# Performance work log

Measured on AMD Instinct MI355X. Metric: run time of the kernel, lower is better.

Reference implementation:

```python
import jax, jax.numpy as jnp
import numpy as np

N_NODE, N_USER = 100000, 30000
N_REL, N_BASIS = 8, 30
EMB, OUT = 32, 32
E = 1600000
BATCH = 16384
H1, H2, H3 = 64, 32, 16
NEG_SLOPE = 0.2


def setup_inputs() -> dict:
    key = jax.random.key(0)
    ks = jax.random.split(key, 20)
    g = lambda k, shape: jax.random.normal(k, shape, dtype=jnp.float32) * 0.05
    inp = {
        "x_ids": jnp.arange(N_NODE, dtype=jnp.int64 if jax.config.jax_enable_x64 else jnp.int32),
        "edge_index": jax.random.randint(ks[0], (2, E), 0, N_NODE),
        "edge_type": jax.random.randint(ks[1], (E,), 0, N_REL),
        "users": jax.random.randint(ks[2], (BATCH,), 0, N_USER),
        "bundles": jax.random.randint(ks[3], (BATCH,), 0, N_NODE),
        # parameters
        "emb": g(ks[4], (N_NODE, EMB)),
        "basis": g(ks[5], (N_BASIS, EMB, OUT)),
        "weight": g(ks[6], (N_REL, N_BASIS)),
        "att": g(ks[7], (N_REL, 2 * OUT)),
        "root": g(ks[8], (EMB, OUT)),
        "bias": jnp.zeros((OUT,), jnp.float32),
        "W1": g(ks[9], (2 * OUT, H1)), "b1": jnp.zeros((H1,), jnp.float32),
        "W2": g(ks[10], (H1, H2)), "b2": jnp.zeros((H2,), jnp.float32),
        "W3": g(ks[11], (H2, H3)), "b3": jnp.zeros((H3,), jnp.float32),
        "Wo": g(ks[12], (H3, 1)), "bo": jnp.zeros((1,), jnp.float32),
    }
    return inp


def _tgcn_fwd(x_ids, edge_index, edge_type, users, bundles,
              emb, basis, weight, att, root, bias,
              W1, b1, W2, b2, W3, b3, Wo, bo):
    N = emb.shape[0]
    R = weight.shape[0]
    O = basis.shape[2]
    x = emb[x_ids]                                   # (N, F) embedding lookup
    # basis decomposition: (R, F, O)
    w = (weight @ basis.reshape(N_BASIS, -1)).reshape(R, EMB, O)
    # transform every node under every relation once, then gather per edge
    xh = jnp.einsum('nf,rfo->nro', x, w)             # (N, R, O)
    src, dst = edge_index[0], edge_index[1]          # j (source), i (target)
    h_i = xh[dst, edge_type]                         # (E, O)
    h_j = xh[src, edge_type]                         # (E, O)
    a = att[edge_type]                               # (E, 2O)
    alpha = (h_i * a[:, :O]).sum(-1) + (h_j * a[:, O:]).sum(-1)
    alpha = jax.nn.leaky_relu(alpha, NEG_SLOPE)
    # segment softmax keyed by (target node, relation)
    seg_key = dst * R + edge_type
    n_seg = N * R
    amax = jax.ops.segment_max(alpha, seg_key, num_segments=n_seg)
    ex = jnp.exp(alpha - amax[seg_key])
    denom = jax.ops.segment_sum(ex, seg_key, num_segments=n_seg)
    alpha = ex / (denom[seg_key] + 1e-16)
    # scatter-add weighted messages into target nodes
    agg = jax.ops.segment_sum(h_j * alpha[:, None], dst, num_segments=N)
    h = jax.nn.relu(agg + x @ root + bias)           # update + ReLU
    z = jnp.concatenate([h[users], h[bundles]], axis=1)  # (B, 2O)
    z = jax.nn.relu(z @ W1 + b1)
    z = jax.nn.relu(z @ W2 + b2)
    z = jax.nn.relu(z @ W3 + b3)
    return z @ Wo + bo                               # (B, 1) logits


def reference(x_ids, edge_index, edge_type, users, bundles,
              emb, basis, weight, att, root, bias,
              W1, b1, W2, b2, W3, b3, Wo, bo):
    return _tgcn_fwd(x_ids, edge_index, edge_type, users, bundles,
                     emb, basis, weight, att, root, bias,
                     W1, b1, W2, b2, W3, b3, Wo, bo)
```

## Files before the change

### kernel.cpp

```cpp
#include <hip/hip_runtime.h>
#include <hip/hip_bf16.h>

#define N_NODE 100000
#define N_REL  8
#define EMB    32
#define OUT    32
#define N_BASIS 30
#define E_EDGE 1600000
#define BATCH  16384
#define H1 64
#define H2 32
#define H3 16
#define NEG_SLOPE 0.2f

#define BSH   8
#define NBKT  391
#define BCAP  5120
#define PCH   2048

#define K5T   128

#define NPB   32
#define NTILES (N_NODE / NPB)
#define K1GRID 782
#define XSS   36
#define RTS   36


__global__ __launch_bounds__(256) void k0f(const float* __restrict__ weight,
                                           const float* __restrict__ basis,
                                           const float* __restrict__ att,
                                           float* __restrict__ w,
                                           float* __restrict__ wa,
                                           unsigned* __restrict__ bcnt) {
    __shared__ float wl[N_REL * EMB * OUT];
    int t = threadIdx.x;
    for (int i = t; i < N_REL * EMB * OUT; i += 256) {
        int r = i >> 10, fo = i & 1023;
        float acc = 0.f;
        #pragma unroll
        for (int b = 0; b < N_BASIS; b++)
            acc = fmaf(weight[r * N_BASIS + b], basis[b * (EMB * OUT) + fo], acc);
        wl[i] = acc;
        w[i] = acc;
    }
    __syncthreads();
    for (int i = t; i < 512; i += 256) {
        int which = i >> 8, rf = i & 255, r = rf >> 5, f = rf & 31;
        const float* wrow = wl + (r * 32 + f) * 32;
        const float* arow = att + r * 64 + which * 32;
        float acc = 0.f;
        #pragma unroll
        for (int o = 0; o < 32; o++) acc = fmaf(wrow[o], arow[o], acc);
        wa[i] = acc;
    }
    for (int i = t; i < NBKT; i += 256) bcnt[i] = 0;
}

__global__ __launch_bounds__(256) void k1x(const float* __restrict__ emb,
                                           const float* __restrict__ w,
                                           const float* __restrict__ wa,
                                           const float* __restrict__ root,
                                           const float* __restrict__ bias,
                                           unsigned short* __restrict__ xh,
                                           float* __restrict__ p_i,
                                           float* __restrict__ p_j,
                                           float* __restrict__ agg) {
    __shared__ float xs[2][NPB * XSS];
    __shared__ float rootsT[OUT * RTS];
    __shared__ float was[16 * RTS];
    __shared__ float biass[OUT];

    const int t = threadIdx.x;
    const int ro = t & 127;
    const int rhi = ro >> 5, olo = ro & 31;

    float wc0[EMB], wc1[EMB];
    #pragma unroll
    for (int f = 0; f < EMB; f++) {
        wc0[f] = w[rhi * 1024 + f * 32 + olo];
        wc1[f] = w[rhi * 1024 + 4096 + f * 32 + olo];
    }
    #pragma unroll
    for (int f = 0; f < EMB; f++) asm volatile("" : "+v"(wc0[f]), "+v"(wc1[f]));

    for (int i = t; i < EMB * OUT; i += 256) {
        int f = i >> 5, oo = i & 31;
        rootsT[oo * RTS + f] = root[i];
    }
    for (int i = t; i < 512; i += 256) {
        int which = i >> 8, r = (i >> 5) & 7, f = i & 31;
        was[(which * 8 + r) * RTS + f] = wa[i];
    }
    if (t < OUT) biass[t] = bias[t];

    const int sn = t >> 3, sc = t & 7;
    int tile = blockIdx.x;
    {
        float4 v = ((const float4*)(emb + (size_t)tile * NPB * EMB))[t];
        *(float4*)&xs[0][sn * XSS + sc * 4] = v;
    }
    __syncthreads();

    int buf = 0;
    for (; tile < NTILES; tile += K1GRID) {
        const int ntile = tile + K1GRID;
        const bool has = ntile < NTILES;
        float4 pf;
        if (has)
            pf = ((const float4*)(emb + (size_t)ntile * NPB * EMB))[t];

        const int n0 = tile * NPB;
        const float* xb = xs[buf];

        {
            const float4* xr = (const float4*)&xb[(t >> 3) * XSS];
            const float4* wi = (const float4*)&was[(t & 7) * RTS];
            const float4* wj = (const float4*)&was[(8 + (t & 7)) * RTS];
            float ai = 0.f, aj = 0.f;
            #pragma unroll
            for (int c = 0; c < 8; c++) {
                float4 xv = xr[c];
                float4 vi = wi[c], vj = wj[c];
                ai = fmaf(xv.x, vi.x, ai); ai = fmaf(xv.y, vi.y, ai);
                ai = fmaf(xv.z, vi.z, ai); ai = fmaf(xv.w, vi.w, ai);
                aj = fmaf(xv.x, vj.x, aj); aj = fmaf(xv.y, vj.y, aj);
                aj = fmaf(xv.z, vj.z, aj); aj = fmaf(xv.w, vj.w, aj);
            }
            p_i[n0 * N_REL + t] = ai;
            p_j[n0 * N_REL + t] = aj;
        }

        {
            const int o = t & 31, ng = t >> 5;
            const float4* rt = (const float4*)&rootsT[o * RTS];
            float4 r0 = rt[0], r1 = rt[1], r2 = rt[2], r3 = rt[3];
            float4 r4 = rt[4], r5 = rt[5], r6 = rt[6], r7 = rt[7];
            float bv = biass[o];
            #pragma unroll
            for (int q = 0; q < 4; q++) {
                int n = ng * 4 + q;
                const float4* xr = (const float4*)&xb[n * XSS];
                float g = bv;
                float4 xv;
                xv = xr[0]; g = fmaf(xv.x, r0.x, g); g = fmaf(xv.y, r0.y, g);
                            g = fmaf(xv.z, r0.z, g); g = fmaf(xv.w, r0.w, g);
                xv = xr[1]; g = fmaf(xv.x, r1.x, g); g = fmaf(xv.y, r1.y, g);
                            g = fmaf(xv.z, r1.z, g); g = fmaf(xv.w, r1.w, g);
                xv = xr[2]; g = fmaf(xv.x, r2.x, g); g = fmaf(xv.y, r2.y, g);
                            g = fmaf(xv.z, r2.z, g); g = fmaf(xv.w, r2.w, g);
                xv = xr[3]; g = fmaf(xv.x, r3.x, g); g = fmaf(xv.y, r3.y, g);
                            g = fmaf(xv.z, r3.z, g); g = fmaf(xv.w, r3.w, g);
                xv = xr[4]; g = fmaf(xv.x, r4.x, g); g = fmaf(xv.y, r4.y, g);
                            g = fmaf(xv.z, r4.z, g); g = fmaf(xv.w, r4.w, g);
                xv = xr[5]; g = fmaf(xv.x, r5.x, g); g = fmaf(xv.y, r5.y, g);
                            g = fmaf(xv.z, r5.z, g); g = fmaf(xv.w, r5.w, g);
                xv = xr[6]; g = fmaf(xv.x, r6.x, g); g = fmaf(xv.y, r6.y, g);
                            g = fmaf(xv.z, r6.z, g); g = fmaf(xv.w, r6.w, g);
                xv = xr[7]; g = fmaf(xv.x, r7.x, g); g = fmaf(xv.y, r7.y, g);
                            g = fmaf(xv.z, r7.z, g); g = fmaf(xv.w, r7.w, g);
                agg[(size_t)(n0 + n) * OUT + o] = g;
            }
        }

        {
            const int half = t >> 7;
            #pragma unroll 4
            for (int s = 0; s < 16; s++) {
                int n = 2 * s + half;
                const float4* xr = (const float4*)&xb[n * XSS];
                float a0 = 0.f, a1 = 0.f;
                #pragma unroll
                for (int c = 0; c < 8; c++) {
                    float4 xv = xr[c];
                    a0 = fmaf(xv.x, wc0[4 * c + 0], a0);
                    a0 = fmaf(xv.y, wc0[4 * c + 1], a0);
                    a0 = fmaf(xv.z, wc0[4 * c + 2], a0);
                    a0 = fmaf(xv.w, wc0[4 * c + 3], a0);
                    a1 = fmaf(xv.x, wc1[4 * c + 0], a1);
                    a1 = fmaf(xv.y, wc1[4 * c + 1], a1);
                    a1 = fmaf(xv.z, wc1[4 * c + 2], a1);
                    a1 = fmaf(xv.w, wc1[4 * c + 3], a1);
                }
                __hip_bfloat16 b0 = __float2bfloat16(a0);
                __hip_bfloat16 b1 = __float2bfloat16(a1);
                unsigned short* xp = xh + (size_t)(n0 + n) * 256;
                xp[ro]       = *(unsigned short*)&b0;
                xp[ro + 128] = *(unsigned short*)&b1;
            }
        }

        if (has)
            *(float4*)&xs[buf ^ 1][sn * XSS + sc * 4] = pf;
        __syncthreads();
        buf ^= 1;
    }
}

__global__ __launch_bounds__(256) void k_part(const int* __restrict__ src,
                                              const int* __restrict__ dst,
                                              const int* __restrict__ et,
                                              unsigned* __restrict__ bcnt,
                                              unsigned* __restrict__ part) {
    __shared__ unsigned long long stage[PCH];
    __shared__ unsigned hist[NBKT], lbase[NBKT], lcur[NBKT], gbase[NBKT];
    __shared__ unsigned sc[256];
    int t = threadIdx.x;
    for (int i = t; i < NBKT; i += 256) hist[i] = 0;
    __syncthreads();
    int beg = blockIdx.x * PCH, end = min(beg + PCH, E_EDGE);
    int n = end - beg;
    int ng = n >> 2;
    int g0 = t, g1 = t + 256;
    bool has0 = g0 < ng, has1 = g1 < ng;
    int4 s0v = {}, d0v = {}, e0v = {}, s1v = {}, d1v = {}, e1v = {};
    if (has0) {
        s0v = *(const int4*)&src[beg + 4 * g0];
        d0v = *(const int4*)&dst[beg + 4 * g0];
        e0v = *(const int4*)&et[beg + 4 * g0];
    }
    if (has1) {
        s1v = *(const int4*)&src[beg + 4 * g1];
        d1v = *(const int4*)&dst[beg + 4 * g1];
        e1v = *(const int4*)&et[beg + 4 * g1];
    }
    if (has0) {
        atomicAdd(&hist[(unsigned)d0v.x >> BSH], 1u);
        atomicAdd(&hist[(unsigned)d0v.y >> BSH], 1u);
        atomicAdd(&hist[(unsigned)d0v.z >> BSH], 1u);
        atomicAdd(&hist[(unsigned)d0v.w >> BSH], 1u);
    }
    if (has1) {
        atomicAdd(&hist[(unsigned)d1v.x >> BSH], 1u);
        atomicAdd(&hist[(unsigned)d1v.y >> BSH], 1u);
        atomicAdd(&hist[(unsigned)d1v.z >> BSH], 1u);
        atomicAdd(&hist[(unsigned)d1v.w >> BSH], 1u);
    }
    __syncthreads();
    unsigned v0 = (2 * t < NBKT) ? hist[2 * t] : 0u;
    unsigned v1 = (2 * t + 1 < NBKT) ? hist[2 * t + 1] : 0u;
    unsigned s = v0 + v1;
    sc[t] = s;
    __syncthreads();
    for (int off = 1; off < 256; off <<= 1) {
        unsigned y = (t >= off) ? sc[t - off] : 0u;
        __syncthreads();
        sc[t] += y;
        __syncthreads();
    }
    unsigned ex = sc[t] - s;
    if (2 * t < NBKT)     { lbase[2 * t] = ex;          lcur[2 * t] = ex; }
    if (2 * t + 1 < NBKT) { lbase[2 * t + 1] = ex + v0; lcur[2 * t + 1] = ex + v0; }
    __syncthreads();
    #define K_PART_STAGE(dd, ss, ee) do {                                   \
        unsigned b_ = (unsigned)(dd) >> BSH;                                \
        unsigned ent_ = ((unsigned)((dd) & 255) << 20)                      \
                      | ((unsigned)(ss) << 3) | (unsigned)(ee);             \
        unsigned pos_ = atomicAdd(&lcur[b_], 1u);                           \
        stage[pos_] = ((unsigned long long)b_ << 32) | ent_; } while (0)
    if (has0) {
        K_PART_STAGE(d0v.x, s0v.x, e0v.x);
        K_PART_STAGE(d0v.y, s0v.y, e0v.y);
        K_PART_STAGE(d0v.z, s0v.z, e0v.z);
        K_PART_STAGE(d0v.w, s0v.w, e0v.w);
    }
    if (has1) {
        K_PART_STAGE(d1v.x, s1v.x, e1v.x);
        K_PART_STAGE(d1v.y, s1v.y, e1v.y);
        K_PART_STAGE(d1v.z, s1v.z, e1v.z);
        K_PART_STAGE(d1v.w, s1v.w, e1v.w);
    }
    #undef K_PART_STAGE
    __syncthreads();
    for (int i = t; i < NBKT; i += 256)
        if (hist[i]) gbase[i] = atomicAdd(&bcnt[i], hist[i]);
    __syncthreads();
    for (int i = t; i < n; i += 256) {
        unsigned long long s64 = stage[i];
        unsigned b = (unsigned)(s64 >> 32);
        unsigned ent = (unsigned)s64;
        part[b * BCAP + gbase[b] + (i - lbase[b])] = ent;
    }
}

__global__ __launch_bounds__(256) void k_sort(const unsigned* __restrict__ bcnt,
                                              const unsigned* __restrict__ part,
                                              int* __restrict__ payload,
                                              int* __restrict__ begp,
                                              int* __restrict__ endp) {
    __shared__ unsigned ent[BCAP];
    __shared__ unsigned ent2[BCAP];
    __shared__ unsigned hist[256], dbase[256], dcur[256];
    __shared__ unsigned sc[256];
    int t = threadIdx.x;
    int b = blockIdx.x;
    unsigned s0 = (unsigned)b * BCAP;
    int n = (int)bcnt[b];
    if (n > BCAP) n = BCAP;
    hist[t] = 0;
    __syncthreads();
    int n4 = n & ~3;
    for (int i = 4 * t; i < n4; i += 1024) {
        uint4 e4 = *(const uint4*)&part[s0 + i];
        ent[i + 0] = e4.x; atomicAdd(&hist[e4.x >> 20], 1u);
        ent[i + 1] = e4.y; atomicAdd(&hist[e4.y >> 20], 1u);
        ent[i + 2] = e4.z; atomicAdd(&hist[e4.z >> 20], 1u);
        ent[i + 3] = e4.w; atomicAdd(&hist[e4.w >> 20], 1u);
    }
    for (int i = n4 + t; i < n; i += 256) {
        unsigned e = part[s0 + i];
        ent[i] = e;
        atomicAdd(&hist[e >> 20], 1u);
    }
    __syncthreads();
    unsigned v = hist[t];
    sc[t] = v;
    __syncthreads();
    for (int off = 1; off < 256; off <<= 1) {
        unsigned y = (t >= off) ? sc[t - off] : 0u;
        __syncthreads();
        sc[t] += y;
        __syncthreads();
    }
    unsigned ex = sc[t] - v;
    dbase[t] = ex;
    dcur[t] = ex;
    __syncthreads();
    int d = (b << BSH) + t;
    if (d < N_NODE) {
        begp[d] = (int)(s0 + dbase[t]);
        endp[d] = (int)(s0 + dbase[t] + hist[t]);
    }
    for (int i = t; i < n; i += 256) {
        unsigned e = ent[i];
        unsigned pos = atomicAdd(&dcur[e >> 20], 1u);
        ent2[pos] = e & 0xFFFFFu;
    }
    __syncthreads();
    for (int i = 4 * t; i < n4; i += 1024) {
        uint4 o4 = { ent2[i + 0], ent2[i + 1], ent2[i + 2], ent2[i + 3] };
        *(uint4*)&payload[s0 + i] = o4;
    }
    for (int i = n4 + t; i < n; i += 256) payload[s0 + i] = (int)ent2[i];
}

__global__ __launch_bounds__(256) void k_agg(const int* __restrict__ begp,
                                             const int* __restrict__ endp,
                                             const int* __restrict__ payload,
                                             const float* __restrict__ p_i,
                                             const float* __restrict__ p_j,
                                             const unsigned short* __restrict__ xh,
                                             float* __restrict__ agg,
                                             int d0, int d1) {
    int d = d0 + blockIdx.x * 4 + (threadIdx.x >> 6);
    if (d >= d1) return;
    const int lane = threadIdx.x & 63;
    const int h = lane >> 5;
    const int o = lane & 31;
    const int beg = begp[d], end = endp[d];
    const int cnt = end - beg;
    if (cnt == 0) return;

    float pid[8];
    #pragma unroll
    for (int k = 0; k < 8; k++) pid[k] = p_i[(d << 3) | k];

    if (cnt <= 64) {
        int sr = 0, r = 0; float ev = 0.f;
        if (lane < cnt) {
            sr = payload[beg + lane];
            r = sr & 7;
            float pi = pid[0];
            #pragma unroll
            for (int k = 1; k < 8; k++) pi = (r == k) ? pid[k] : pi;
            float a = pi + p_j[sr];
            a = (a >= 0.f) ? a : NEG_SLOPE * a;
            ev = __expf(a);
        }
        float sex[8];
        #pragma unroll
        for (int k = 0; k < 8; k++) sex[k] = (r == k) ? ev : 0.f;
        #pragma unroll
        for (int k = 0; k < 8; k++) {
            #pragma unroll
            for (int m = 1; m <= 32; m <<= 1) sex[k] += __shfl_xor(sex[k], m, 64);
        }
        float de = sex[0];
        #pragma unroll
        for (int k = 1; k < 8; k++) de = (r == k) ? sex[k] : de;
        float al = ev / (de + 1e-16f);

        float w0 = 0.f, w1 = 0.f, w2 = 0.f, w3 = 0.f;
        for (int j0 = 0; j0 < cnt; j0 += 8) {
            float b0 = __shfl(al, j0 + h,     64);
            float b1 = __shfl(al, j0 + 2 + h, 64);
            float b2 = __shfl(al, j0 + 4 + h, 64);
            float b3 = __shfl(al, j0 + 6 + h, 64);
            int t0 = payload[beg + j0 + h]     & 0xFFFFF;
            int t1 = payload[beg + j0 + 2 + h] & 0xFFFFF;
            int t2 = payload[beg + j0 + 4 + h] & 0xFFFFF;
            int t3 = payload[beg + j0 + 6 + h] & 0xFFFFF;
            float x0 = __uint_as_float((unsigned)xh[((unsigned)t0 << 5) + o] << 16);
            float x1 = __uint_as_float((unsigned)xh[((unsigned)t1 << 5) + o] << 16);
            float x2 = __uint_as_float((unsigned)xh[((unsigned)t2 << 5) + o] << 16);
            float x3 = __uint_as_float((unsigned)xh[((unsigned)t3 << 5) + o] << 16);
            w0 = fmaf(b0, x0, w0); w1 = fmaf(b1, x1, w1);
            w2 = fmaf(b2, x2, w2); w3 = fmaf(b3, x3, w3);
        }
        float vv = (w0 + w1) + (w2 + w3);
        vv += __shfl_xor(vv, 32, 64);
        if (h == 0) agg[(size_t)d * OUT + o] += vv;
        return;
    }

    float sex[8] = {0.f,0.f,0.f,0.f,0.f,0.f,0.f,0.f};
    for (int i = beg + lane; i < end; i += 64) {
        int sr = payload[i];
        int r = sr & 7;
        float pi = pid[0];
        #pragma unroll
        for (int k = 1; k < 8; k++) pi = (r == k) ? pid[k] : pi;
        float a = pi + p_j[sr];
        a = (a >= 0.f) ? a : NEG_SLOPE * a;
        float ev = __expf(a);
        #pragma unroll
        for (int k = 0; k < 8; k++) sex[k] += (r == k) ? ev : 0.f;
    }
    #pragma unroll
    for (int k = 0; k < 8; k++) {
        #pragma unroll
        for (int m = 1; m <= 32; m <<= 1) sex[k] += __shfl_xor(sex[k], m, 64);
    }
    float v0 = 0.f;
    for (int c = beg; c < end; c += 64) {
        int i = c + lane;
        int sr = 0; float al = 0.f;
        if (i < end) {
            sr = payload[i];
            int r = sr & 7;
            float pi = pid[0];
            #pragma unroll
            for (int k = 1; k < 8; k++) pi = (r == k) ? pid[k] : pi;
            float a = pi + p_j[sr];
            a = (a >= 0.f) ? a : NEG_SLOPE * a;
            float ev = __expf(a);
            float de = sex[0];
            #pragma unroll
            for (int k = 1; k < 8; k++) de = (r == k) ? sex[k] : de;
            al = ev / (de + 1e-16f);
        }
        int m = min(64, end - c);
        for (int j0 = 0; j0 < m; j0 += 2) {
            int e0 = j0 + h;
            float a0 = __shfl(al, e0, 64); int s0 = __shfl(sr, e0, 64);
            if (e0 < m) {
                float xv = __uint_as_float((unsigned)xh[((unsigned)s0 << 5) + o] << 16);
                v0 = fmaf(a0, xv, v0);
            }
        }
    }
    float vv = v0;
    vv += __shfl_xor(vv, 32, 64);
    if (h == 0) agg[(size_t)d * OUT + o] += vv;
}

__global__ __launch_bounds__(K5T, 1) void k5_mlp(const int* __restrict__ users,
                                                 const int* __restrict__ bundles,
                                                 const float* __restrict__ agg,
                                                 const float* __restrict__ W1,
                                                 const float* __restrict__ b1,
                                                 const float* __restrict__ W2,
                                                 const float* __restrict__ b2,
                                                 const float* __restrict__ W3,
                                                 const float* __restrict__ b3,
                                                 const float* __restrict__ Wo,
                                                 const float* __restrict__ bo,
                                                 float* __restrict__ out) {
    __shared__ float4 W1s[2 * OUT * H1 / 4];
    __shared__ float4 W2s[H1 * H2 / 4];
    __shared__ float4 W3s[H2 * H3 / 4];
    __shared__ float b1s[H1], b2s[H2], b3s[H3], Wos[H3];
    __shared__ float bos;
    __shared__ float zs[K5T * 65];
    __shared__ float h1s[K5T * 65];
    const int t = threadIdx.x;

    const float4* W14 = (const float4*)W1;
    const float4* W24 = (const float4*)W2;
    const float4* W34 = (const float4*)W3;
    for (int i = t; i < 1024; i += K5T) W1s[i] = W14[i];
    for (int i = t; i < 512; i += K5T) W2s[i] = W24[i];
    for (int i = t; i < 128; i += K5T) W3s[i] = W34[i];
    if (t < H1) b1s[t] = b1[t];
    if (t < H2) b2s[t] = b2[t];
    if (t < H3) { b3s[t] = b3[t]; Wos[t] = Wo[t]; }
    if (t == 0) bos = bo[0];

    const int item = blockIdx.x * K5T + t;
    const int u = users[item], v = bundles[item];
    const float4* av = (const float4*)agg;
    float* zrow = &zs[t * 65];
    float* h1row = &h1s[t * 65];

    #pragma unroll
    for (int c = 0; c < 8; c++) {
        float4 x = av[(size_t)u * 8 + c];
        zrow[4 * c + 0] = fmaxf(x.x, 0.f); zrow[4 * c + 1] = fmaxf(x.y, 0.f);
        zrow[4 * c + 2] = fmaxf(x.z, 0.f); zrow[4 * c + 3] = fmaxf(x.w, 0.f);
    }
    #pragma unroll
    for (int c = 0; c < 8; c++) {
        float4 x = av[(size_t)v * 8 + c];
        zrow[32 + 4 * c + 0] = fmaxf(x.x, 0.f); zrow[32 + 4 * c + 1] = fmaxf(x.y, 0.f);
        zrow[32 + 4 * c + 2] = fmaxf(x.z, 0.f); zrow[32 + 4 * c + 3] = fmaxf(x.w, 0.f);
    }
    __syncthreads();

    #pragma unroll 4
    for (int j4 = 0; j4 < 16; j4++) {
        float a0 = b1s[4 * j4 + 0], a1 = b1s[4 * j4 + 1];
        float a2 = b1s[4 * j4 + 2], a3 = b1s[4 * j4 + 3];
        #pragma unroll 16
        for (int k = 0; k < 2 * OUT; k++) {
            float zk = zrow[k];
            float4 wv = W1s[k * 16 + j4];
            a0 = fmaf(zk, wv.x, a0); a1 = fmaf(zk, wv.y, a1);
            a2 = fmaf(zk, wv.z, a2); a3 = fmaf(zk, wv.w, a3);
        }
        h1row[4 * j4 + 0] = fmaxf(a0, 0.f); h1row[4 * j4 + 1] = fmaxf(a1, 0.f);
        h1row[4 * j4 + 2] = fmaxf(a2, 0.f); h1row[4 * j4 + 3] = fmaxf(a3, 0.f);
    }

    #pragma unroll 4
    for (int j4 = 0; j4 < 8; j4++) {
        float a0 = b2s[4 * j4 + 0], a1 = b2s[4 * j4 + 1];
        float a2 = b2s[4 * j4 + 2], a3 = b2s[4 * j4 + 3];
        #pragma unroll 16
        for (int k = 0; k < H1; k++) {
            float hk = h1row[k];
            float4 wv = W2s[k * 8 + j4];
            a0 = fmaf(hk, wv.x, a0); a1 = fmaf(hk, wv.y, a1);
            a2 = fmaf(hk, wv.z, a2); a3 = fmaf(hk, wv.w, a3);
        }
        zrow[4 * j4 + 0] = fmaxf(a0, 0.f); zrow[4 * j4 + 1] = fmaxf(a1, 0.f);
        zrow[4 * j4 + 2] = fmaxf(a2, 0.f); zrow[4 * j4 + 3] = fmaxf(a3, 0.f);
    }

    float h3v[16];
    #pragma unroll
    for (int j4 = 0; j4 < 4; j4++) {
        float a0 = b3s[4 * j4 + 0], a1 = b3s[4 * j4 + 1];
        float a2 = b3s[4 * j4 + 2], a3 = b3s[4 * j4 + 3];
        #pragma unroll 16
        for (int k = 0; k < H2; k++) {
            float hk = zrow[k];
            float4 wv = W3s[k * 4 + j4];
            a0 = fmaf(hk, wv.x, a0); a1 = fmaf(hk, wv.y, a1);
            a2 = fmaf(hk, wv.z, a2); a3 = fmaf(hk, wv.w, a3);
        }
        h3v[4 * j4 + 0] = fmaxf(a0, 0.f); h3v[4 * j4 + 1] = fmaxf(a1, 0.f);
        h3v[4 * j4 + 2] = fmaxf(a2, 0.f); h3v[4 * j4 + 3] = fmaxf(a3, 0.f);
    }

    float acc = bos;
    #pragma unroll
    for (int k = 0; k < H3; k++) acc = fmaf(h3v[k], Wos[k], acc);
    out[item] = acc;
}

extern "C" void kernel_launch(void* const* d_in, const int* in_sizes, int n_in,
                              void* d_out, int out_size, void* d_ws, size_t ws_size,
                              hipStream_t stream) {
    (void)in_sizes; (void)n_in; (void)out_size; (void)ws_size;
    const int*   eidx   = (const int*)d_in[1];
    const int*   etype  = (const int*)d_in[2];
    const int*   users  = (const int*)d_in[3];
    const int*   bund   = (const int*)d_in[4];
    const float* emb    = (const float*)d_in[5];
    const float* basis  = (const float*)d_in[6];
    const float* weight = (const float*)d_in[7];
    const float* att    = (const float*)d_in[8];
    const float* root   = (const float*)d_in[9];
    const float* bias   = (const float*)d_in[10];
    const float* W1 = (const float*)d_in[11]; const float* b1 = (const float*)d_in[12];
    const float* W2 = (const float*)d_in[13]; const float* b2 = (const float*)d_in[14];
    const float* W3 = (const float*)d_in[15]; const float* b3 = (const float*)d_in[16];
    const float* Wo = (const float*)d_in[17]; const float* bo = (const float*)d_in[18];
    float* out = (float*)d_out;

    const int* src = eidx;
    const int* dst = eidx + E_EDGE;

    float* ws       = (float*)d_ws;
    float* w        = ws;
    float* wa       = w + N_REL * EMB * OUT;
    unsigned short* xh = (unsigned short*)(wa + 512);
    float* p_i      = (float*)(xh + (size_t)N_NODE * 256);
    float* p_j      = p_i + N_NODE * N_REL;
    float* agg      = p_j + N_NODE * N_REL;
    int*   payload  = (int*)(agg + (long)N_NODE * OUT);
    int*   begp     = payload + NBKT * BCAP;
    int*   endp     = begp + N_NODE;
    unsigned* bcnt  = (unsigned*)(endp + N_NODE);
    unsigned* part  = (unsigned*)agg;

    k0f<<<1, 256, 0, stream>>>(weight, basis, att, w, wa, bcnt);
    k_part<<<(E_EDGE + PCH - 1) / PCH, 256, 0, stream>>>(src, dst, etype, bcnt, part);
    k_sort<<<NBKT, 256, 0, stream>>>(bcnt, part, payload, begp, endp);
    k1x<<<K1GRID, 256, 0, stream>>>(emb, w, wa, root, bias, xh, p_i, p_j, agg);
    k_agg<<<12500, 256, 0, stream>>>(begp, endp, payload, p_i, p_j, xh, agg,
                                     0, 50000);
    k_agg<<<12500, 256, 0, stream>>>(begp, endp, payload, p_i, p_j, xh, agg,
                                     50000, 100000);
    k5_mlp<<<BATCH / K5T, K5T, 0, stream>>>(users, bund, agg, W1, b1, W2, b2, W3, b3,
                                            Wo, bo, out);
}
```

Before: 316.8 us.

## Fuse sort and node-transform kernels into one launch with separate partition buffer

Moves the partition scratch buffer out of the agg region when the workspace is large enough. That removes the aliasing hazard, so the bucket sort and the node transform can run concurrently as one heterogeneous grid with a shared-memory union. It also merges the two half-range aggregation launches into a single launch and halves the MLP block size. The gain is fewer launches and overlap of two independent stages, at the cost of a larger shared-memory footprint for the transform blocks and extra workspace use.

```diff
diff --git a/kernel.cpp b/kernel.cpp
--- a/kernel.cpp
+++ b/kernel.cpp
@@ -18,7 +18,7 @@
 #define BCAP  5120
 #define PCH   2048
 
-#define K5T   128
+#define K5T   64
 
 #define NPB   32
 #define NTILES (N_NODE / NPB)
@@ -26,6 +26,18 @@
 #define XSS   36
 #define RTS   36
 
+
+struct SortSmem {
+    unsigned ent[BCAP];
+    unsigned ent2[BCAP];
+    unsigned hist[256], dbase[256], dcur[256], sc[256];
+};
+struct K1Smem {
+    float xs[2][NPB * XSS];
+    float rootsT[OUT * RTS];
+    float was[16 * RTS];
+    float biass[OUT];
+};
 
 __global__ __launch_bounds__(256) void k0f(const float* __restrict__ weight,
                                            const float* __restrict__ basis,
@@ -57,20 +69,16 @@
     for (int i = t; i < NBKT; i += 256) bcnt[i] = 0;
 }
 
-__global__ __launch_bounds__(256) void k1x(const float* __restrict__ emb,
-                                           const float* __restrict__ w,
-                                           const float* __restrict__ wa,
-                                           const float* __restrict__ root,
-                                           const float* __restrict__ bias,
-                                           unsigned short* __restrict__ xh,
-                                           float* __restrict__ p_i,
-                                           float* __restrict__ p_j,
-                                           float* __restrict__ agg) {
-    __shared__ float xs[2][NPB * XSS];
-    __shared__ float rootsT[OUT * RTS];
-    __shared__ float was[16 * RTS];
-    __shared__ float biass[OUT];
-
+__device__ __forceinline__ void k1x_body(K1Smem& K, int bid0,
+                                         const float* __restrict__ emb,
+                                         const float* __restrict__ w,
+                                         const float* __restrict__ wa,
+                                         const float* __restrict__ root,
+                                         const float* __restrict__ bias,
+                                         unsigned short* __restrict__ xh,
+                                         float* __restrict__ p_i,
+                                         float* __restrict__ p_j,
+                                         float* __restrict__ agg) {
     const int t = threadIdx.x;
     const int ro = t & 127;
     const int rhi = ro >> 5, olo = ro & 31;
@@ -86,19 +94,19 @@
 
     for (int i = t; i < EMB * OUT; i += 256) {
         int f = i >> 5, oo = i & 31;
-        rootsT[oo * RTS + f] = root[i];
+        K.rootsT[oo * RTS + f] = root[i];
     }
     for (int i = t; i < 512; i += 256) {
         int which = i >> 8, r = (i >> 5) & 7, f = i & 31;
-        was[(which * 8 + r) * RTS + f] = wa[i];
-    }
-    if (t < OUT) biass[t] = bias[t];
-
-    const int sn = t >> 3, sc = t & 7;
-    int tile = blockIdx.x;
+        K.was[(which * 8 + r) * RTS + f] = wa[i];
+    }
+    if (t < OUT) K.biass[t] = bias[t];
+
+    const int sn = t >> 3, scn = t & 7;
+    int tile = bid0;
     {
         float4 v = ((const float4*)(emb + (size_t)tile * NPB * EMB))[t];
-        *(float4*)&xs[0][sn * XSS + sc * 4] = v;
+        *(float4*)&K.xs[0][sn * XSS + scn * 4] = v;
     }
     __syncthreads();
 
@@ -111,12 +119,12 @@
             pf = ((const float4*)(emb + (size_t)ntile * NPB * EMB))[t];
 
         const int n0 = tile * NPB;
-        const float* xb = xs[buf];
+        const float* xb = K.xs[buf];
 
         {
             const float4* xr = (const float4*)&xb[(t >> 3) * XSS];
-            const float4* wi = (const float4*)&was[(t & 7) * RTS];
-            const float4* wj = (const float4*)&was[(8 + (t & 7)) * RTS];
+            const float4* wi = (const float4*)&K.was[(t & 7) * RTS];
+            const float4* wj = (const float4*)&K.was[(8 + (t & 7)) * RTS];
             float ai = 0.f, aj = 0.f;
             #pragma unroll
             for (int c = 0; c < 8; c++) {
@@ -133,10 +141,10 @@
 
         {
             const int o = t & 31, ng = t >> 5;
-            const float4* rt = (const float4*)&rootsT[o * RTS];
+            const float4* rt = (const float4*)&K.rootsT[o * RTS];
             float4 r0 = rt[0], r1 = rt[1], r2 = rt[2], r3 = rt[3];
             float4 r4 = rt[4], r5 = rt[5], r6 = rt[6], r7 = rt[7];
-            float bv = biass[o];
+            float bv = K.biass[o];
             #pragma unroll
             for (int q = 0; q < 4; q++) {
                 int n = ng * 4 + q;
@@ -191,10 +199,110 @@
         }
 
         if (has)
-            *(float4*)&xs[buf ^ 1][sn * XSS + sc * 4] = pf;
+            *(float4*)&K.xs[buf ^ 1][sn * XSS + scn * 4] = pf;
         __syncthreads();
         buf ^= 1;
     }
+}
+
+__device__ __forceinline__ void sort_body(SortSmem& S, int b,
+                                          const unsigned* __restrict__ bcnt,
+                                          const unsigned* __restrict__ part,
+                                          int* __restrict__ payload,
+                                          int* __restrict__ begp,
+                                          int* __restrict__ endp) {
+    int t = threadIdx.x;
+    unsigned s0 = (unsigned)b * BCAP;
+    int n = (int)bcnt[b];
+    if (n > BCAP) n = BCAP;
+    S.hist[t] = 0;
+    __syncthreads();
+    int n4 = n & ~3;
+    for (int i = 4 * t; i < n4; i += 1024) {
+        uint4 e4 = *(const uint4*)&part[s0 + i];
+        S.ent[i + 0] = e4.x; atomicAdd(&S.hist[e4.x >> 20], 1u);
+        S.ent[i + 1] = e4.y; atomicAdd(&S.hist[e4.y >> 20], 1u);
+        S.ent[i + 2] = e4.z; atomicAdd(&S.hist[e4.z >> 20], 1u);
+        S.ent[i + 3] = e4.w; atomicAdd(&S.hist[e4.w >> 20], 1u);
+    }
+    for (int i = n4 + t; i < n; i += 256) {
+        unsigned e = part[s0 + i];
+        S.ent[i] = e;
+        atomicAdd(&S.hist[e >> 20], 1u);
+    }
+    __syncthreads();
+    unsigned v = S.hist[t];
+    S.sc[t] = v;
+    __syncthreads();
+    for (int off = 1; off < 256; off <<= 1) {
+        unsigned y = (t >= off) ? S.sc[t - off] : 0u;
+        __syncthreads();
+        S.sc[t] += y;
+        __syncthreads();
+    }
+    unsigned ex = S.sc[t] - v;
+    S.dbase[t] = ex;
+    S.dcur[t] = ex;
+    __syncthreads();
+    int d = (b << BSH) + t;
+    if (d < N_NODE) {
+        begp[d] = (int)(s0 + S.dbase[t]);
+        endp[d] = (int)(s0 + S.dbase[t] + S.hist[t]);
+    }
+    for (int i = t; i < n; i += 256) {
+        unsigned e = S.ent[i];
+        unsigned pos = atomicAdd(&S.dcur[e >> 20], 1u);
+        S.ent2[pos] = e & 0xFFFFFu;
+    }
+    __syncthreads();
+    for (int i = 4 * t; i < n4; i += 1024) {
+        uint4 o4 = { S.ent2[i + 0], S.ent2[i + 1], S.ent2[i + 2], S.ent2[i + 3] };
+        *(uint4*)&payload[s0 + i] = o4;
+    }
+    for (int i = n4 + t; i < n; i += 256) payload[s0 + i] = (int)S.ent2[i];
+}
+
+__global__ __launch_bounds__(256) void k1x(const float* __restrict__ emb,
+                                           const float* __restrict__ w,
+                                           const float* __restrict__ wa,
+                                           const float* __restrict__ root,
+                                           const float* __restrict__ bias,
+                                           unsigned short* __restrict__ xh,
+                                           float* __restrict__ p_i,
+                                           float* __restrict__ p_j,
+                                           float* __restrict__ agg) {
+    __shared__ K1Smem K;
+    k1x_body(K, blockIdx.x, emb, w, wa, root, bias, xh, p_i, p_j, agg);
+}
+
+__global__ __launch_bounds__(256) void k_sort(const unsigned* __restrict__ bcnt,
+                                              const unsigned* __restrict__ part,
+                                              int* __restrict__ payload,
+                                              int* __restrict__ begp,
+                                              int* __restrict__ endp) {
+    __shared__ SortSmem S;
+    sort_body(S, blockIdx.x, bcnt, part, payload, begp, endp);
+}
+
+__global__ __launch_bounds__(256) void k_sx(const unsigned* __restrict__ bcnt,
+                                            const unsigned* __restrict__ part,
+                                            int* __restrict__ payload,
+                                            int* __restrict__ begp,
+                                            int* __restrict__ endp,
+                                            const float* __restrict__ emb,
+                                            const float* __restrict__ w,
+                                            const float* __restrict__ wa,
+                                            const float* __restrict__ root,
+                                            const float* __restrict__ bias,
+                                            unsigned short* __restrict__ xh,
+                                            float* __restrict__ p_i,
+                                            float* __restrict__ p_j,
+                                            float* __restrict__ agg) {
+    __shared__ union USmem { SortSmem s; K1Smem k; } u;
+    if (blockIdx.x < K1GRID)
+        k1x_body(u.k, blockIdx.x, emb, w, wa, root, bias, xh, p_i, p_j, agg);
+    else
+        sort_body(u.s, blockIdx.x - K1GRID, bcnt, part, payload, begp, endp);
 }
 
 __global__ __launch_bounds__(256) void k_part(const int* __restrict__ src,
@@ -281,67 +389,6 @@
         unsigned ent = (unsigned)s64;
         part[b * BCAP + gbase[b] + (i - lbase[b])] = ent;
     }
-}
-
-__global__ __launch_bounds__(256) void k_sort(const unsigned* __restrict__ bcnt,
-                                              const unsigned* __restrict__ part,
-                                              int* __restrict__ payload,
-                                              int* __restrict__ begp,
-                                              int* __restrict__ endp) {
-    __shared__ unsigned ent[BCAP];
-    __shared__ unsigned ent2[BCAP];
-    __shared__ unsigned hist[256], dbase[256], dcur[256];
-    __shared__ unsigned sc[256];
-    int t = threadIdx.x;
-    int b = blockIdx.x;
-    unsigned s0 = (unsigned)b * BCAP;
-    int n = (int)bcnt[b];
-    if (n > BCAP) n = BCAP;
-    hist[t] = 0;
-    __syncthreads();
-    int n4 = n & ~3;
-    for (int i = 4 * t; i < n4; i += 1024) {
-        uint4 e4 = *(const uint4*)&part[s0 + i];
-        ent[i + 0] = e4.x; atomicAdd(&hist[e4.x >> 20], 1u);
-        ent[i + 1] = e4.y; atomicAdd(&hist[e4.y >> 20], 1u);
-        ent[i + 2] = e4.z; atomicAdd(&hist[e4.z >> 20], 1u);
-        ent[i + 3] = e4.w; atomicAdd(&hist[e4.w >> 20], 1u);
-    }
-    for (int i = n4 + t; i < n; i += 256) {
-        unsigned e = part[s0 + i];
-        ent[i] = e;
-        atomicAdd(&hist[e >> 20], 1u);
-    }
-    __syncthreads();
-    unsigned v = hist[t];
-    sc[t] = v;
-    __syncthreads();
-    for (int off = 1; off < 256; off <<= 1) {
-        unsigned y = (t >= off) ? sc[t - off] : 0u;
-        __syncthreads();
-        sc[t] += y;
-        __syncthreads();
-    }
-    unsigned ex = sc[t] - v;
-    dbase[t] = ex;
-    dcur[t] = ex;
-    __syncthreads();
-    int d = (b << BSH) + t;
-    if (d < N_NODE) {
-        begp[d] = (int)(s0 + dbase[t]);
-        endp[d] = (int)(s0 + dbase[t] + hist[t]);
-    }
-    for (int i = t; i < n; i += 256) {
-        unsigned e = ent[i];
-        unsigned pos = atomicAdd(&dcur[e >> 20], 1u);
-        ent2[pos] = e & 0xFFFFFu;
-    }
-    __syncthreads();
-    for (int i = 4 * t; i < n4; i += 1024) {
-        uint4 o4 = { ent2[i + 0], ent2[i + 1], ent2[i + 2], ent2[i + 3] };
-        *(uint4*)&payload[s0 + i] = o4;
-    }
-    for (int i = n4 + t; i < n; i += 256) payload[s0 + i] = (int)ent2[i];
 }
 
 __global__ __launch_bounds__(256) void k_agg(const int* __restrict__ begp,
@@ -491,9 +538,9 @@
     for (int i = t; i < 1024; i += K5T) W1s[i] = W14[i];
     for (int i = t; i < 512; i += K5T) W2s[i] = W24[i];
     for (int i = t; i < 128; i += K5T) W3s[i] = W34[i];
-    if (t < H1) b1s[t] = b1[t];
     if (t < H2) b2s[t] = b2[t];
     if (t < H3) { b3s[t] = b3[t]; Wos[t] = Wo[t]; }
+    if (t < H1) b1s[t] = b1[t];
     if (t == 0) bos = bo[0];
 
     const int item = blockIdx.x * K5T + t;
@@ -571,7 +618,7 @@
 extern "C" void kernel_launch(void* const* d_in, const int* in_sizes, int n_in,
                               void* d_out, int out_size, void* d_ws, size_t ws_size,
                               hipStream_t stream) {
-    (void)in_sizes; (void)n_in; (void)out_size; (void)ws_size;
+    (void)in_sizes; (void)n_in; (void)out_size;
     const int*   eidx   = (const int*)d_in[1];
     const int*   etype  = (const int*)d_in[2];
     const int*   users  = (const int*)d_in[3];
@@ -598,20 +645,28 @@
     float* p_i      = (float*)(xh + (size_t)N_NODE * 256);
     float* p_j      = p_i + N_NODE * N_REL;
     float* agg      = p_j + N_NODE * N_REL;
-    int*   payload  = (int*)(agg + (long)N_NODE * OUT);
-    int*   begp     = payload + NBKT * BCAP;
+    int*   payload  = (int*)(agg + (size_t)N_NODE * OUT);
+    int*   begp     = payload + (size_t)NBKT * BCAP;
     int*   endp     = begp + N_NODE;
     unsigned* bcnt  = (unsigned*)(endp + N_NODE);
-    unsigned* part  = (unsigned*)agg;
+    unsigned* part_sep = bcnt + 512;
+    size_t needed = (size_t)((char*)(part_sep + (size_t)NBKT * BCAP) - (char*)d_ws);
+
+    const bool fused = ws_size >= needed;
+    unsigned* part = fused ? part_sep : (unsigned*)agg;
 
     k0f<<<1, 256, 0, stream>>>(weight, basis, att, w, wa, bcnt);
     k_part<<<(E_EDGE + PCH - 1) / PCH, 256, 0, stream>>>(src, dst, etype, bcnt, part);
-    k_sort<<<NBKT, 256, 0, stream>>>(bcnt, part, payload, begp, endp);
-    k1x<<<K1GRID, 256, 0, stream>>>(emb, w, wa, root, bias, xh, p_i, p_j, agg);
-    k_agg<<<12500, 256, 0, stream>>>(begp, endp, payload, p_i, p_j, xh, agg,
-                                     0, 50000);
-    k_agg<<<12500, 256, 0, stream>>>(begp, endp, payload, p_i, p_j, xh, agg,
-                                     50000, 100000);
+    if (fused) {
+        k_sx<<<K1GRID + NBKT, 256, 0, stream>>>(bcnt, part, payload, begp, endp,
+                                                emb, w, wa, root, bias,
+                                                xh, p_i, p_j, agg);
+    } else {
+        k_sort<<<NBKT, 256, 0, stream>>>(bcnt, part, payload, begp, endp);
+        k1x<<<K1GRID, 256, 0, stream>>>(emb, w, wa, root, bias, xh, p_i, p_j, agg);
+    }
+    k_agg<<<N_NODE / 4, 256, 0, stream>>>(begp, endp, payload, p_i, p_j, xh, agg,
+                                          0, N_NODE);
     k5_mlp<<<BATCH / K5T, K5T, 0, stream>>>(users, bund, agg, W1, b1, W2, b2, W3, b3,
                                             Wo, bo, out);
 }
```

Measured after the change: 300.9 us. -5.0%, faster.
